# Kernel optimization log

Measured on AMD Instinct MI355X. Metric: run time of the kernel, lower is better.

Reference implementation:

```python
import jax, jax.numpy as jnp
import numpy as np

KS = 3          # deformable kernel size
N = KS * KS     # sampling points per output location


def conv2d(x, w, stride, pad):
    return jax.lax.conv_general_dilated(
        x, w, (stride, stride), [(pad, pad), (pad, pad)],
        dimension_numbers=('NCHW', 'OIHW', 'NCHW'))


def bn_train(x, g, b, eps=1e-5):
    # training-mode BatchNorm2d: per-channel batch statistics (biased var)
    m = jnp.mean(x, axis=(0, 2, 3), keepdims=True)
    v = jnp.var(x, axis=(0, 2, 3), keepdims=True)
    return (x - m) * jax.lax.rsqrt(v + eps) * g.reshape(1, -1, 1, 1) + b.reshape(1, -1, 1, 1)


def gather_xq(xpad, qx, qy):
    # xpad: (b,c,Hp,Wp); qx,qy: (b,h,w,N) int32 -> (b,c,h,w,N)
    b, c, Hp, Wp = xpad.shape
    _, h, w, n = qx.shape
    idx = (qx * Wp + qy).reshape(b, 1, h * w * n)
    xf = xpad.reshape(b, c, Hp * Wp)
    out = jnp.take_along_axis(xf, jnp.broadcast_to(idx, (b, c, h * w * n)), axis=2)
    return out.reshape(b, c, h, w, n)


def deform_conv(x, Wp, bp, Wd):
    # self-contained DeformConv2D (deform-conv-v2 style, no modulation)
    b, c, h, w = x.shape
    offset = conv2d(x, Wp, 1, 1) + bp.reshape(1, -1, 1, 1)      # (b,2N,h,w)
    off = jnp.transpose(offset, (0, 2, 3, 1))                    # (b,h,w,2N)
    xpad = jnp.pad(x, ((0, 0), (0, 0), (1, 1), (1, 1)))          # zero_padding(1)
    Hpad, Wpad = h + 2, w + 2
    r = KS // 2
    pn_x = jnp.repeat(jnp.arange(-r, r + 1, dtype=x.dtype), KS)  # [-1,-1,-1,0,0,0,1,1,1]
    pn_y = jnp.tile(jnp.arange(-r, r + 1, dtype=x.dtype), KS)    # [-1,0,1,...]
    # sampling coords in padded image: p = p0 + pn + offset
    px = off[..., :N] + jnp.arange(1, h + 1, dtype=x.dtype)[None, :, None, None] + pn_x
    py = off[..., N:] + jnp.arange(1, w + 1, dtype=x.dtype)[None, None, :, None] + pn_y
    fx = jnp.floor(jax.lax.stop_gradient(px))
    fy = jnp.floor(jax.lax.stop_gradient(py))
    q_ltx = jnp.clip(fx, 0, Hpad - 1).astype(jnp.int32)
    q_lty = jnp.clip(fy, 0, Wpad - 1).astype(jnp.int32)
    q_rbx = jnp.clip(fx + 1, 0, Hpad - 1).astype(jnp.int32)
    q_rby = jnp.clip(fy + 1, 0, Wpad - 1).astype(jnp.int32)
    pxc = jnp.clip(px, 0, Hpad - 1)
    pyc = jnp.clip(py, 0, Wpad - 1)
    g_lt = (1 + (q_ltx - pxc)) * (1 + (q_lty - pyc))
    g_rb = (1 - (q_rbx - pxc)) * (1 - (q_rby - pyc))
    g_lb = (1 + (q_ltx - pxc)) * (1 - (q_rby - pyc))
    g_rt = (1 - (q_rbx - pxc)) * (1 + (q_lty - pyc))
    x_off = (g_lt[:, None] * gather_xq(xpad, q_ltx, q_lty)
           + g_rb[:, None] * gather_xq(xpad, q_rbx, q_rby)
           + g_lb[:, None] * gather_xq(xpad, q_ltx, q_rby)
           + g_rt[:, None] * gather_xq(xpad, q_rbx, q_lty))    # (b,c,h,w,N)
    # _reshape_x_offset: (b,c,h,w,kx,ky) -> (b,c,h*ks,w*ks)
    x_off = x_off.reshape(b, c, h, w, KS, KS).transpose(0, 1, 2, 4, 3, 5).reshape(b, c, h * KS, w * KS)
    return conv2d(x_off, Wd, KS, 0)                              # stride=ks conv


def setup_inputs() -> dict:
    key = jax.random.key(0)
    ks = jax.random.split(key, 8)
    def w(k, shape, fan):
        return jax.random.normal(k, shape, jnp.float32) * np.float32(1.0 / np.sqrt(fan))
    B = 2048
    return dict(
        x=jax.random.normal(ks[0], (B, 3, 4, 4), jnp.float32),
        W1=w(ks[1], (32, 3, 3, 3), 27),
        g1=jnp.ones(32, jnp.float32), b1=jnp.zeros(32, jnp.float32),
        W2=w(ks[2], (64, 32, 3, 3), 288),
        g2=jnp.ones(64, jnp.float32), b2=jnp.zeros(64, jnp.float32),
        W3=w(ks[3], (128, 64, 3, 3), 576),
        g3=jnp.ones(128, jnp.float32), b3=jnp.zeros(128, jnp.float32),
        Wp=w(ks[4], (18, 128, 3, 3), 1152) * np.float32(0.1),
        bp=jnp.zeros(18, jnp.float32),
        Wd=w(ks[5], (128, 128, 3, 3), 1152),
        g4=jnp.ones(128, jnp.float32), b4=jnp.zeros(128, jnp.float32),
        Wc=w(ks[6], (10, 128), 128),
        bc=jnp.zeros(10, jnp.float32),
    )


def reference(x, W1, g1, b1, W2, g2, b2, W3, g3, b3, Wp, bp, Wd, g4, b4, Wc, bc):
    x = bn_train(jax.nn.relu(conv2d(x, W1, 1, 1)), g1, b1)
    x = bn_train(jax.nn.relu(conv2d(x, W2, 1, 1)), g2, b2)
    x = bn_train(jax.nn.relu(conv2d(x, W3, 1, 1)), g3, b3)
    x = bn_train(jax.nn.relu(deform_conv(x, Wp, bp, Wd)), g4, b4)
    x = jnp.mean(x, axis=(2, 3))  # avg_pool2d(kernel=4) on 4x4 -> 1x1, then flatten
    return x @ Wc.T + bc
```

## Files before the change

### kernel.cpp

```cpp
#include <hip/hip_runtime.h>

#define NB 2048
#define CNT 32768.0f

#define OFF_Y1   0
#define OFF_Y2   524288
#define OFF_Y3   1572864
#define OFF_MEAN 3670016
#define OFF_ST   3932160
#define OFF_W2P  3933184
#define OFF_W3P  3942400
#define OFF_WPP  3979264
#define OFF_WDP  3997696

typedef __attribute__((ext_vector_type(8))) short bf16x8;
typedef __attribute__((ext_vector_type(4))) float f32x4;

__device__ __forceinline__ unsigned short f2bf(float f) {
  union { float f; unsigned int u; } v; v.f = f;
  unsigned int r = v.u + 0x7FFFu + ((v.u >> 16) & 1u);
  return (unsigned short)(r >> 16);
}
__device__ __forceinline__ float bf2f(unsigned short u) {
  union { unsigned int u; float f; } v; v.u = ((unsigned int)u) << 16;
  return v.f;
}

__device__ __forceinline__ void packw_one(const float* __restrict__ w, unsigned short* __restrict__ wpk,
                                          int CI, int CO, int NT, int i) {
  int KST = CI >> 5;
  int j = i & 7, l = (i >> 3) & 63, sn = i >> 9;
  int nt = sn % NT, step = sn / NT;
  int tap = step / KST, ks = step - tap * KST;
  int ci = ks * 32 + (l >> 4) * 8 + j, co = nt * 16 + (l & 15);
  wpk[i] = (co < CO) ? f2bf(w[(co * CI + ci) * 9 + tap]) : (unsigned short)0;
}

__device__ __forceinline__ void packwd_one(const float* __restrict__ Wd, unsigned short* __restrict__ wdp, int i) {
  int co = i / 1152, k = i % 1152;
  int tt = k >> 5, kk = k & 31, g = kk >> 3, j = kk & 7;
  int n = k >> 7, ci = k & 127;
  int nt = co >> 4, cc = co & 15, l = g * 16 + cc;
  wdp[((tt * 8 + nt) * 64 + l) * 8 + j] = f2bf(Wd[co * 1152 + ci * 9 + n]);
}

__global__ __launch_bounds__(256) void k_pre(const float* __restrict__ W2, const float* __restrict__ W3,
                                             const float* __restrict__ Wp, const float* __restrict__ Wd,
                                             unsigned short* __restrict__ w2p, unsigned short* __restrict__ w3p,
                                             unsigned short* __restrict__ wpp, unsigned short* __restrict__ wdp,
                                             const float* __restrict__ x, const float* __restrict__ W1,
                                             unsigned short* __restrict__ y1, float* __restrict__ st) {
  __shared__ float xs[384];
  __shared__ float w1s[864];
  __shared__ float sst[64];
  int t = threadIdx.x;
  if (blockIdx.x < 270) {
#pragma unroll
    for (int ii = 0; ii < 4; ++ii) {
      int i = blockIdx.x * 1024 + ii * 256 + t;
      if (i < 18432) packw_one(W2, w2p, 32, 64, 4, i);
      else if (i < 92160) packw_one(W3, w3p, 64, 128, 8, i - 18432);
      else if (i < 129024) packw_one(Wp, wpp, 128, 18, 2, i - 92160);
      else if (i < 276480) packwd_one(Wd, wdp, i - 129024);
    }
    return;
  }
  int b0 = (blockIdx.x - 270) * 8;
  if (t < 128) { xs[t] = x[b0 * 48 + t]; xs[256 + t] = x[b0 * 48 + 256 + t]; }
  else if (t < 256) xs[t] = x[b0 * 48 + t];
  for (int i = t; i < 864; i += 256) w1s[i] = W1[i];
  if (t < 64) sst[t] = 0.f;
  __syncthreads();
  for (int r = 0; r < 2; ++r) {
    int o = t + r * 256;
    int co = o >> 4, p = o & 15, h = p >> 2, w = p & 3;
    float s1 = 0.f, s2 = 0.f;
#pragma unroll
    for (int img = 0; img < 8; ++img) {
      float acc = 0.f;
      for (int ci = 0; ci < 3; ++ci) {
#pragma unroll
        for (int kx = 0; kx < 3; ++kx) {
          int ih = h + kx - 1;
          if (ih < 0 || ih > 3) continue;
#pragma unroll
          for (int ky = 0; ky < 3; ++ky) {
            int iw = w + ky - 1;
            if (iw < 0 || iw > 3) continue;
            acc += w1s[co * 27 + ci * 9 + kx * 3 + ky] * xs[img * 48 + ci * 16 + ih * 4 + iw];
          }
        }
      }
      acc = fmaxf(acc, 0.f);
      y1[(b0 + img) * 512 + o] = f2bf(acc);
      s1 += acc; s2 += acc * acc;
    }
    atomicAdd(&sst[co], s1);
    atomicAdd(&sst[32 + co], s2);
  }
  __syncthreads();
  if (t < 64) atomicAdd(&st[(t < 32) ? t : (96 + t)], sst[t]);
}

template <int CI, int CO>
__global__ __launch_bounds__(512, 4) void k_convm(const unsigned short* __restrict__ yin,
                                                  const unsigned short* __restrict__ wpk,
                                                  const float* __restrict__ stp,
                                                  const float* __restrict__ gp,
                                                  const float* __restrict__ bpar,
                                                  unsigned short* __restrict__ yout, float* __restrict__ stout) {
  constexpr int KST = CI / 32, NSTEP = 9 * KST, NT = CO / 16;
  constexpr int STR = (CI == 64) ? 72 : 40;
  constexpr int NCH = (NT == 8) ? 8 : 4;
  __shared__ __align__(16) unsigned short xnT[8][36 * STR];
  __shared__ float cst[4][CO * 16];
  __shared__ float scS[2 * CI];
  __shared__ float sst[2 * CO];
  int b0 = blockIdx.x * 8, t = threadIdx.x;
  uint4 z = {0u, 0u, 0u, 0u};
  for (int i = t; i < (8 * 36 * STR) / 8; i += 512) ((uint4*)xnT)[i] = z;
  if (t < CI) {
    float m = stp[t] / CNT;
    float v = stp[128 + t] / CNT - m * m;
    float s = gp[t] * rsqrtf(fmaxf(v, 0.f) + 1e-5f);
    scS[t] = s; scS[CI + t] = bpar[t] - m * s;
  }
  if (t < 2 * CO) sst[t] = 0.f;
  __syncthreads();
  for (int i = t; i < 8 * CI * 16; i += 512) {
    int img = i / (CI * 16), r = i - img * (CI * 16);
    int c = r >> 4, p = r & 15, h = p >> 2, w = p & 3;
    float v = bf2f(yin[(b0 + img) * CI * 16 + r]) * scS[c] + scS[CI + c];
    xnT[img][((h + 1) * 6 + (w + 1)) * STR + c] = f2bf(v);
  }
  __syncthreads();
  int wv = t >> 6, l = t & 63, px = l & 15, g = l >> 4, cc = l & 15;
  int h = px >> 2, w = px & 3;
  int wq = (NT == 8) ? wv : (wv & 3);
  int ib = (NT == 8) ? 0 : ((wv >> 2) * 4);
  f32x4 acc[NCH];
#pragma unroll
  for (int e = 0; e < NCH; ++e) acc[e] = f32x4{0.f, 0.f, 0.f, 0.f};
#pragma unroll
  for (int step = 0; step < NSTEP; ++step) {
    int tap = step / KST, ks = step - tap * KST;
    int kx = tap / 3, ky = tap % 3;
    bf16x8 bb = *(const bf16x8*)&wpk[((step * NT + wq) * 64 + l) * 8];
    int woff = ((h + kx) * 6 + (w + ky)) * STR + ks * 32 + g * 8;
#pragma unroll
    for (int e = 0; e < NCH; ++e) {
      bf16x8 a = *(const bf16x8*)&xnT[ib + e][woff];
      acc[e] = __builtin_amdgcn_mfma_f32_16x16x32_bf16(a, bb, acc[e], 0, 0, 0);
    }
  }
#pragma unroll
  for (int p = 0; p < 2; ++p) {
    if (NT == 8) {
#pragma unroll
      for (int e = 0; e < 4; ++e) {
        int co = wq * 16 + cc;
#pragma unroll
        for (int r = 0; r < 4; ++r) cst[e][co * 16 + (g * 4 + r)] = acc[4 * p + e][r];
      }
    } else {
      if ((wv >> 2) == p) {
#pragma unroll
        for (int e = 0; e < 4; ++e) {
          int co = wq * 16 + cc;
#pragma unroll
          for (int r = 0; r < 4; ++r) cst[e][co * 16 + (g * 4 + r)] = acc[e][r];
        }
      }
    }
    __syncthreads();
    if (NT == 8) {
      int ime = t >> 7, c = t & 127;
      float s1 = 0.f, s2 = 0.f;
      union { unsigned short u16[16]; uint4 u4[2]; } pk;
#pragma unroll
      for (int e = 0; e < 16; ++e) {
        float v = fmaxf(cst[ime][c * 16 + e], 0.f);
        pk.u16[e] = f2bf(v);
        s1 += v; s2 += v * v;
      }
      unsigned short* dst = &yout[(b0 + 4 * p + ime) * CO * 16 + c * 16];
      *(uint4*)dst = pk.u4[0];
      *(uint4*)(dst + 8) = pk.u4[1];
      atomicAdd(&sst[c], s1);
      atomicAdd(&sst[CO + c], s2);
    } else {
      int ime = t >> 7, tl = t & 127;
      int c = tl >> 1, e0 = (t & 1) * 8;
      float s1 = 0.f, s2 = 0.f;
      union { unsigned short u16[8]; uint4 u4; } pk;
#pragma unroll
      for (int e = 0; e < 8; ++e) {
        float v = fmaxf(cst[ime][c * 16 + e0 + e], 0.f);
        pk.u16[e] = f2bf(v);
        s1 += v; s2 += v * v;
      }
      *(uint4*)&yout[(b0 + 4 * p + ime) * CO * 16 + c * 16 + e0] = pk.u4;
      atomicAdd(&sst[c], s1);
      atomicAdd(&sst[CO + c], s2);
    }
    __syncthreads();
  }
  if (t < 2 * CO) atomicAdd(&stout[(t < CO) ? t : (128 - CO + t)], sst[t]);
}

__global__ __launch_bounds__(512, 4) void k_deform(const unsigned short* __restrict__ y3,
                                                   const unsigned short* __restrict__ wppk,
                                                   const float* __restrict__ bp,
                                                   const unsigned short* __restrict__ wdp,
                                                   const float* __restrict__ stp,
                                                   const float* __restrict__ gp,
                                                   const float* __restrict__ bpar,
                                                   float* __restrict__ meanw, float* __restrict__ stout) {
  __shared__ __align__(16) unsigned char smem[51712];
  unsigned short* xnb2 = (unsigned short*)smem;
  unsigned short* xnT  = (unsigned short*)(smem + 8192);
  unsigned short* sAT  = (unsigned short*)(smem + 8192);
  unsigned short* xoffA = (unsigned short*)(smem + 31232);
  float* cscr = (float*)(smem + 31232);
  float* scS  = (float*)(smem + 49664);
  float* sst  = (float*)(smem + 50688);
  int b0 = blockIdx.x * 2, t = threadIdx.x;
  uint4 z = {0u, 0u, 0u, 0u};
  for (int i = t; i < 1224; i += 512) ((uint4*)xnT)[i] = z;
  if (t < 128) {
    float m = stp[t] / CNT;
    float v = stp[128 + t] / CNT - m * m;
    float s = gp[t] * rsqrtf(fmaxf(v, 0.f) + 1e-5f);
    scS[t] = s; scS[128 + t] = bpar[t] - m * s;
  }
  if (t < 256) sst[t] = 0.f;
  __syncthreads();
  for (int i = t; i < 4096; i += 512) {
    int img = i >> 11, r = i & 2047;
    int c = r >> 4, p = r & 15, h = p >> 2, w = p & 3;
    float v = bf2f(y3[(b0 + img) * 2048 + r]) * scS[c] + scS[128 + c];
    unsigned short bv = f2bf(v);
    xnb2[img * 2048 + c * 16 + p] = bv;
    xnT[img * 4896 + ((h + 1) * 6 + (w + 1)) * 136 + c] = bv;
  }
  __syncthreads();
  int wv = t >> 6, l = t & 63, px = l & 15, g = l >> 4, cc = l & 15;
  int h = px >> 2, w = px & 3;
  {
    int imo = wv >> 2, half = (wv >> 1) & 1, nt = wv & 1;
    f32x4 oa = {0.f, 0.f, 0.f, 0.f};
#pragma unroll
    for (int si = 0; si < 18; ++si) {
      int s2 = half * 18 + si;
      int tap = s2 >> 2, ks = s2 & 3;
      int kx = tap / 3, ky = tap % 3;
      bf16x8 a = *(const bf16x8*)&xnT[imo * 4896 + ((h + kx) * 6 + (w + ky)) * 136 + ks * 32 + g * 8];
      bf16x8 bb = *(const bf16x8*)&wppk[((s2 * 2 + nt) * 64 + l) * 8];
      oa = __builtin_amdgcn_mfma_f32_16x16x32_bf16(a, bb, oa, 0, 0, 0);
    }
#pragma unroll
    for (int r = 0; r < 4; ++r) cscr[wv * 256 + (g * 4 + r) * 16 + px] = oa[r];
  }
  __syncthreads();
  if (t < 288) {
    int imo = t / 144, r = t - imo * 144;
    int p = r / 9, n = r % 9;
    int hh = p >> 2, ww = p & 3;
    int o1 = n, o2 = 9 + n;
    int nt1 = o1 >> 4, c1 = o1 & 15;
    int nt2 = o2 >> 4, c2 = o2 & 15;
    float off1 = bp[o1] + cscr[(imo * 4 + nt1) * 256 + p * 16 + c1]
               + cscr[(imo * 4 + 2 + nt1) * 256 + p * 16 + c1];
    float off2 = bp[o2] + cscr[(imo * 4 + nt2) * 256 + p * 16 + c2]
               + cscr[(imo * 4 + 2 + nt2) * 256 + p * 16 + c2];
    float sx = off1 + (float)(hh + 1) + (float)(n / 3 - 1);
    float sy = off2 + (float)(ww + 1) + (float)(n % 3 - 1);
    float fx = floorf(sx), fy = floorf(sy);
    float qlx = fminf(fmaxf(fx, 0.f), 5.f);
    float qly = fminf(fmaxf(fy, 0.f), 5.f);
    float qrx = fminf(fmaxf(fx + 1.f, 0.f), 5.f);
    float qry = fminf(fmaxf(fy + 1.f, 0.f), 5.f);
    float pxc = fminf(fmaxf(sx, 0.f), 5.f);
    float pyc = fminf(fmaxf(sy, 0.f), 5.f);
    float glt = (1.f + (qlx - pxc)) * (1.f + (qly - pyc));
    float grb = (1.f - (qrx - pxc)) * (1.f - (qry - pyc));
    float glb = (1.f + (qlx - pxc)) * (1.f - (qry - pyc));
    float grt = (1.f - (qrx - pxc)) * (1.f + (qly - pyc));
    int ilx = (int)qlx, ily = (int)qly, irx = (int)qrx, iry = (int)qry;
    int rowb = imo * 5760 + (n * 16 + p) * 40;
    uint4* rp = (uint4*)&sAT[rowb];
    rp[0] = z; rp[1] = z; rp[2] = z; rp[3] = z; rp[4] = z;
    auto PUT = [&](int qx, int qy, float gv) {
      if (qx >= 1 && qx <= 4 && qy >= 1 && qy <= 4)
        sAT[rowb + (qx - 1) * 4 + (qy - 1)] = f2bf(gv);
    };
    PUT(ilx, ily, glt);
    PUT(irx, iry, grb);
    PUT(ilx, iry, glb);
    PUT(irx, ily, grt);
  }
  __syncthreads();
  f32x4 acc0 = {0.f, 0.f, 0.f, 0.f};
  f32x4 acc1 = {0.f, 0.f, 0.f, 0.f};
  for (int ph = 0; ph < 4; ++ph) {
    for (int m = wv; m < 36; m += 8) {
      int imo = m / 18, mm = m - imo * 18;
      int ttl = mm >> 1;
      int tt = ph * 9 + ttl;
      int q = tt & 3, n = tt >> 2;
      int ct = 2 * q + (mm & 1);
      bf16x8 a = *(const bf16x8*)&xnb2[imo * 2048 + (ct * 16 + cc) * 16 + g * 8];
      bf16x8 bS = *(const bf16x8*)&sAT[imo * 5760 + (n * 16 + cc) * 40 + g * 8];
      f32x4 d = __builtin_amdgcn_mfma_f32_16x16x32_bf16(a, bS, f32x4{0.f, 0.f, 0.f, 0.f}, 0, 0, 0);
      int gp2 = (ct & 1) * 2 + (g >> 1);
      unsigned lo = (unsigned)f2bf(d[0]) | ((unsigned)f2bf(d[1]) << 16);
      unsigned hi = (unsigned)f2bf(d[2]) | ((unsigned)f2bf(d[3]) << 16);
      *(uint2*)&xoffA[imo * 4608 + (ttl * 64 + gp2 * 16 + cc) * 8 + (g & 1) * 4] = (uint2){lo, hi};
    }
    __syncthreads();
    __builtin_amdgcn_s_setprio(1);
#pragma unroll
    for (int ti = 0; ti < 9; ++ti) {
      bf16x8 bb = *(const bf16x8*)&wdp[(((ph * 9 + ti) * 8 + wv) * 64 + l) * 8];
      bf16x8 a0 = *(const bf16x8*)&xoffA[(ti * 64 + l) * 8];
      bf16x8 a1 = *(const bf16x8*)&xoffA[4608 + (ti * 64 + l) * 8];
      acc0 = __builtin_amdgcn_mfma_f32_16x16x32_bf16(a0, bb, acc0, 0, 0, 0);
      acc1 = __builtin_amdgcn_mfma_f32_16x16x32_bf16(a1, bb, acc1, 0, 0, 0);
    }
    __builtin_amdgcn_s_setprio(0);
    __syncthreads();
  }
  {
    float s1a = 0.f, s2a = 0.f, s1b = 0.f, s2b = 0.f;
#pragma unroll
    for (int r = 0; r < 4; ++r) {
      float v0 = fmaxf(acc0[r], 0.f);
      float v1 = fmaxf(acc1[r], 0.f);
      s1a += v0; s2a += v0 * v0;
      s1b += v1; s2b += v1 * v1;
    }
    s1a += __shfl_xor(s1a, 16); s1a += __shfl_xor(s1a, 32);
    s2a += __shfl_xor(s2a, 16); s2a += __shfl_xor(s2a, 32);
    s1b += __shfl_xor(s1b, 16); s1b += __shfl_xor(s1b, 32);
    s2b += __shfl_xor(s2b, 16); s2b += __shfl_xor(s2b, 32);
    if (g == 0) {
      int co = wv * 16 + cc;
      meanw[b0 * 128 + co] = s1a;
      meanw[(b0 + 1) * 128 + co] = s1b;
      atomicAdd(&sst[co], s1a + s1b);
      atomicAdd(&sst[128 + co], s2a + s2b);
    }
  }
  __syncthreads();
  if (t < 256) atomicAdd(&stout[t], sst[t]);
}

__global__ __launch_bounds__(256) void k_final(const float* __restrict__ mean,
                                               const float* __restrict__ stp,
                                               const float* __restrict__ gp,
                                               const float* __restrict__ bpar,
                                               const float* __restrict__ Wc, const float* __restrict__ bc,
                                               float* __restrict__ out) {
  __shared__ float wf[1280];
  __shared__ float scS[256];
  __shared__ float tb[10];
  int t = threadIdx.x;
  if (t < 128) {
    float m = stp[t] / CNT;
    float v = stp[128 + t] / CNT - m * m;
    float s = gp[t] * rsqrtf(fmaxf(v, 0.f) + 1e-5f);
    scS[t] = s; scS[128 + t] = bpar[t] - m * s;
  }
  __syncthreads();
  for (int i = t; i < 1280; i += 256) {
    int c = i & 127;
    wf[i] = Wc[i] * scS[c] * 0.0625f;
  }
  __syncthreads();
  if (t < 10) {
    float s = bc[t];
    for (int c = 0; c < 128; ++c) s += Wc[t * 128 + c] * scS[128 + c];
    tb[t] = s;
  }
  __syncthreads();
  int gidx = blockIdx.x * 256 + t;
  int img = gidx / 10, o = gidx - img * 10;
  const float* mr = mean + img * 128;
  const float* wr = wf + o * 128;
  float acc = tb[o];
#pragma unroll 8
  for (int c = 0; c < 128; ++c) acc += wr[c] * mr[c];
  out[gidx] = acc;
}

extern "C" void kernel_launch(void* const* d_in, const int* in_sizes, int n_in,
                              void* d_out, int out_size, void* d_ws, size_t ws_size,
                              hipStream_t stream) {
  const float* x  = (const float*)d_in[0];
  const float* W1 = (const float*)d_in[1];
  const float* g1 = (const float*)d_in[2];
  const float* b1 = (const float*)d_in[3];
  const float* W2 = (const float*)d_in[4];
  const float* g2 = (const float*)d_in[5];
  const float* b2 = (const float*)d_in[6];
  const float* W3 = (const float*)d_in[7];
  const float* g3 = (const float*)d_in[8];
  const float* b3 = (const float*)d_in[9];
  const float* Wp = (const float*)d_in[10];
  const float* bp = (const float*)d_in[11];
  const float* Wd = (const float*)d_in[12];
  const float* g4 = (const float*)d_in[13];
  const float* b4 = (const float*)d_in[14];
  const float* Wc = (const float*)d_in[15];
  const float* bc = (const float*)d_in[16];
  float* ws = (float*)d_ws;
  float* out = (float*)d_out;

  hipMemsetAsync(ws + OFF_ST, 0, 1024 * sizeof(float), stream);
  k_pre<<<526, 256, 0, stream>>>(W2, W3, Wp, Wd,
                                 (unsigned short*)(ws + OFF_W2P), (unsigned short*)(ws + OFF_W3P),
                                 (unsigned short*)(ws + OFF_WPP), (unsigned short*)(ws + OFF_WDP),
                                 x, W1, (unsigned short*)(ws + OFF_Y1), ws + OFF_ST);
  k_convm<32, 64><<<NB / 8, 512, 0, stream>>>((const unsigned short*)(ws + OFF_Y1),
                                              (const unsigned short*)(ws + OFF_W2P),
                                              ws + OFF_ST, g1, b1,
                                              (unsigned short*)(ws + OFF_Y2), ws + OFF_ST + 256);
  k_convm<64, 128><<<NB / 8, 512, 0, stream>>>((const unsigned short*)(ws + OFF_Y2),
                                               (const unsigned short*)(ws + OFF_W3P),
                                               ws + OFF_ST + 256, g2, b2,
                                               (unsigned short*)(ws + OFF_Y3), ws + OFF_ST + 512);
  k_deform<<<NB / 2, 512, 0, stream>>>((const unsigned short*)(ws + OFF_Y3),
                                       (const unsigned short*)(ws + OFF_WPP), bp,
                                       (const unsigned short*)(ws + OFF_WDP),
                                       ws + OFF_ST + 512, g3, b3, ws + OFF_MEAN, ws + OFF_ST + 768);
  k_final<<<80, 256, 0, stream>>>(ws + OFF_MEAN, ws + OFF_ST + 768, g4, b4, Wc, bc, out);
}
```

Measured before the change: 120.1 us.

## Split deform conv into offset kernel and GEMM kernel with 4 images per block

The fused deformable-conv kernel is split into two kernels. k_offs normalizes y3, computes offsets and bilinear sampling matrices for 4 images per block, and writes the normalized activations and sampling matrices to global workspace. k_dgemm reloads them and runs the deformable GEMM on 4 images per block, so each Wd weight fragment is reused across 4 accumulators instead of 2. The goal is to cut weight-load traffic per image and free LDS, at the cost of an extra global round trip for the intermediates and one more launch.

```diff
diff --git a/kernel.cpp b/kernel.cpp
--- a/kernel.cpp
+++ b/kernel.cpp
@@ -6,12 +6,14 @@
 #define OFF_Y1   0
 #define OFF_Y2   524288
 #define OFF_Y3   1572864
-#define OFF_MEAN 3670016
-#define OFF_ST   3932160
-#define OFF_W2P  3933184
-#define OFF_W3P  3942400
-#define OFF_WPP  3979264
-#define OFF_WDP  3997696
+#define OFF_XNB  3670016
+#define OFF_SAT  5767168
+#define OFF_MEAN 10485760
+#define OFF_ST   10747904
+#define OFF_W2P  10748928
+#define OFF_W3P  10758144
+#define OFF_WPP  10795008
+#define OFF_WDP  10813440
 
 typedef __attribute__((ext_vector_type(8))) short bf16x8;
 typedef __attribute__((ext_vector_type(4))) float f32x4;
@@ -208,73 +210,64 @@
   if (t < 2 * CO) atomicAdd(&stout[(t < CO) ? t : (128 - CO + t)], sst[t]);
 }
 
-__global__ __launch_bounds__(512, 4) void k_deform(const unsigned short* __restrict__ y3,
-                                                   const unsigned short* __restrict__ wppk,
-                                                   const float* __restrict__ bp,
-                                                   const unsigned short* __restrict__ wdp,
-                                                   const float* __restrict__ stp,
-                                                   const float* __restrict__ gp,
-                                                   const float* __restrict__ bpar,
-                                                   float* __restrict__ meanw, float* __restrict__ stout) {
-  __shared__ __align__(16) unsigned char smem[51712];
-  unsigned short* xnb2 = (unsigned short*)smem;
-  unsigned short* xnT  = (unsigned short*)(smem + 8192);
-  unsigned short* sAT  = (unsigned short*)(smem + 8192);
-  unsigned short* xoffA = (unsigned short*)(smem + 31232);
-  float* cscr = (float*)(smem + 31232);
-  float* scS  = (float*)(smem + 49664);
-  float* sst  = (float*)(smem + 50688);
-  int b0 = blockIdx.x * 2, t = threadIdx.x;
+__global__ __launch_bounds__(512, 4) void k_offs(const unsigned short* __restrict__ y3,
+                                                 const unsigned short* __restrict__ wppk,
+                                                 const float* __restrict__ bp,
+                                                 const float* __restrict__ stp,
+                                                 const float* __restrict__ gp,
+                                                 const float* __restrict__ bpar,
+                                                 unsigned short* __restrict__ xnbG,
+                                                 unsigned short* __restrict__ satG) {
+  __shared__ __align__(16) unsigned char smem[44800];
+  unsigned short* xnT = (unsigned short*)smem;
+  float* offs = (float*)(smem + 39168);
+  float* scS  = (float*)(smem + 43776);
+  int b0 = blockIdx.x * 4, t = threadIdx.x;
   uint4 z = {0u, 0u, 0u, 0u};
-  for (int i = t; i < 1224; i += 512) ((uint4*)xnT)[i] = z;
+  for (int i = t; i < 2448; i += 512) ((uint4*)xnT)[i] = z;
   if (t < 128) {
     float m = stp[t] / CNT;
     float v = stp[128 + t] / CNT - m * m;
     float s = gp[t] * rsqrtf(fmaxf(v, 0.f) + 1e-5f);
     scS[t] = s; scS[128 + t] = bpar[t] - m * s;
   }
-  if (t < 256) sst[t] = 0.f;
-  __syncthreads();
-  for (int i = t; i < 4096; i += 512) {
+  __syncthreads();
+  for (int i = t; i < 8192; i += 512) {
     int img = i >> 11, r = i & 2047;
     int c = r >> 4, p = r & 15, h = p >> 2, w = p & 3;
-    float v = bf2f(y3[(b0 + img) * 2048 + r]) * scS[c] + scS[128 + c];
+    float v = bf2f(y3[b0 * 2048 + i]) * scS[c] + scS[128 + c];
     unsigned short bv = f2bf(v);
-    xnb2[img * 2048 + c * 16 + p] = bv;
     xnT[img * 4896 + ((h + 1) * 6 + (w + 1)) * 136 + c] = bv;
+    xnbG[b0 * 2048 + i] = bv;
   }
   __syncthreads();
   int wv = t >> 6, l = t & 63, px = l & 15, g = l >> 4, cc = l & 15;
   int h = px >> 2, w = px & 3;
   {
-    int imo = wv >> 2, half = (wv >> 1) & 1, nt = wv & 1;
+    int img = wv >> 1, nt = wv & 1;
     f32x4 oa = {0.f, 0.f, 0.f, 0.f};
 #pragma unroll
-    for (int si = 0; si < 18; ++si) {
-      int s2 = half * 18 + si;
+    for (int s2 = 0; s2 < 36; ++s2) {
       int tap = s2 >> 2, ks = s2 & 3;
       int kx = tap / 3, ky = tap % 3;
-      bf16x8 a = *(const bf16x8*)&xnT[imo * 4896 + ((h + kx) * 6 + (w + ky)) * 136 + ks * 32 + g * 8];
+      bf16x8 a = *(const bf16x8*)&xnT[img * 4896 + ((h + kx) * 6 + (w + ky)) * 136 + ks * 32 + g * 8];
       bf16x8 bb = *(const bf16x8*)&wppk[((s2 * 2 + nt) * 64 + l) * 8];
       oa = __builtin_amdgcn_mfma_f32_16x16x32_bf16(a, bb, oa, 0, 0, 0);
     }
-#pragma unroll
-    for (int r = 0; r < 4; ++r) cscr[wv * 256 + (g * 4 + r) * 16 + px] = oa[r];
-  }
-  __syncthreads();
-  if (t < 288) {
-    int imo = t / 144, r = t - imo * 144;
+    int o = nt * 16 + cc;
+    if (o < 18) {
+      float bo = bp[o];
+#pragma unroll
+      for (int r = 0; r < 4; ++r) offs[img * 288 + o * 16 + (g * 4 + r)] = oa[r] + bo;
+    }
+  }
+  __syncthreads();
+  for (int s = t; s < 576; s += 512) {
+    int imo = s / 144, r = s - imo * 144;
     int p = r / 9, n = r % 9;
     int hh = p >> 2, ww = p & 3;
-    int o1 = n, o2 = 9 + n;
-    int nt1 = o1 >> 4, c1 = o1 & 15;
-    int nt2 = o2 >> 4, c2 = o2 & 15;
-    float off1 = bp[o1] + cscr[(imo * 4 + nt1) * 256 + p * 16 + c1]
-               + cscr[(imo * 4 + 2 + nt1) * 256 + p * 16 + c1];
-    float off2 = bp[o2] + cscr[(imo * 4 + nt2) * 256 + p * 16 + c2]
-               + cscr[(imo * 4 + 2 + nt2) * 256 + p * 16 + c2];
-    float sx = off1 + (float)(hh + 1) + (float)(n / 3 - 1);
-    float sy = off2 + (float)(ww + 1) + (float)(n % 3 - 1);
+    float sx = offs[imo * 288 + n * 16 + p] + (float)(hh + 1) + (float)(n / 3 - 1);
+    float sy = offs[imo * 288 + (9 + n) * 16 + p] + (float)(ww + 1) + (float)(n % 3 - 1);
     float fx = floorf(sx), fy = floorf(sy);
     float qlx = fminf(fmaxf(fx, 0.f), 5.f);
     float qly = fminf(fmaxf(fy, 0.f), 5.f);
@@ -287,30 +280,48 @@
     float glb = (1.f + (qlx - pxc)) * (1.f - (qry - pyc));
     float grt = (1.f - (qrx - pxc)) * (1.f + (qly - pyc));
     int ilx = (int)qlx, ily = (int)qly, irx = (int)qrx, iry = (int)qry;
-    int rowb = imo * 5760 + (n * 16 + p) * 40;
-    uint4* rp = (uint4*)&sAT[rowb];
-    rp[0] = z; rp[1] = z; rp[2] = z; rp[3] = z; rp[4] = z;
+    unsigned short* row = &satG[((b0 + imo) * 144 + (n * 16 + p)) * 32];
+    uint4* rp = (uint4*)row;
+    rp[0] = z; rp[1] = z; rp[2] = z; rp[3] = z;
     auto PUT = [&](int qx, int qy, float gv) {
       if (qx >= 1 && qx <= 4 && qy >= 1 && qy <= 4)
-        sAT[rowb + (qx - 1) * 4 + (qy - 1)] = f2bf(gv);
+        row[(qx - 1) * 4 + (qy - 1)] = f2bf(gv);
     };
     PUT(ilx, ily, glt);
     PUT(irx, iry, grb);
     PUT(ilx, iry, glb);
     PUT(irx, ily, grt);
   }
-  __syncthreads();
-  f32x4 acc0 = {0.f, 0.f, 0.f, 0.f};
-  f32x4 acc1 = {0.f, 0.f, 0.f, 0.f};
+}
+
+__global__ __launch_bounds__(512, 4) void k_dgemm(const unsigned short* __restrict__ xnbG,
+                                                  const unsigned short* __restrict__ satG,
+                                                  const unsigned short* __restrict__ wdp,
+                                                  float* __restrict__ meanw, float* __restrict__ stout) {
+  __shared__ __align__(16) unsigned char smem[54336];
+  unsigned short* xnb2 = (unsigned short*)smem;
+  unsigned short* xoffA = (unsigned short*)(smem + 16416);
+  float* sst = (float*)(smem + 53312);
+  int b0 = blockIdx.x * 4, t = threadIdx.x;
+  uint4 z = {0u, 0u, 0u, 0u};
+  if (t < 256) sst[t] = 0.f;
+  if (t < 2) ((uint4*)(smem + 16384))[t] = z;
+  for (int i = t; i < 1024; i += 512)
+    ((uint4*)xnb2)[i] = ((const uint4*)&xnbG[b0 * 2048])[i];
+  __syncthreads();
+  int wv = t >> 6, l = t & 63, g = l >> 4, cc = l & 15;
+  f32x4 acc[4];
+#pragma unroll
+  for (int e = 0; e < 4; ++e) acc[e] = f32x4{0.f, 0.f, 0.f, 0.f};
   for (int ph = 0; ph < 4; ++ph) {
-    for (int m = wv; m < 36; m += 8) {
+    for (int m = wv; m < 72; m += 8) {
       int imo = m / 18, mm = m - imo * 18;
       int ttl = mm >> 1;
       int tt = ph * 9 + ttl;
       int q = tt & 3, n = tt >> 2;
       int ct = 2 * q + (mm & 1);
       bf16x8 a = *(const bf16x8*)&xnb2[imo * 2048 + (ct * 16 + cc) * 16 + g * 8];
-      bf16x8 bS = *(const bf16x8*)&sAT[imo * 5760 + (n * 16 + cc) * 40 + g * 8];
+      bf16x8 bS = *(const bf16x8*)&satG[((b0 + imo) * 144 + (n * 16 + cc)) * 32 + g * 8];
       f32x4 d = __builtin_amdgcn_mfma_f32_16x16x32_bf16(a, bS, f32x4{0.f, 0.f, 0.f, 0.f}, 0, 0, 0);
       int gp2 = (ct & 1) * 2 + (g >> 1);
       unsigned lo = (unsigned)f2bf(d[0]) | ((unsigned)f2bf(d[1]) << 16);
@@ -322,33 +333,38 @@
 #pragma unroll
     for (int ti = 0; ti < 9; ++ti) {
       bf16x8 bb = *(const bf16x8*)&wdp[(((ph * 9 + ti) * 8 + wv) * 64 + l) * 8];
-      bf16x8 a0 = *(const bf16x8*)&xoffA[(ti * 64 + l) * 8];
-      bf16x8 a1 = *(const bf16x8*)&xoffA[4608 + (ti * 64 + l) * 8];
-      acc0 = __builtin_amdgcn_mfma_f32_16x16x32_bf16(a0, bb, acc0, 0, 0, 0);
-      acc1 = __builtin_amdgcn_mfma_f32_16x16x32_bf16(a1, bb, acc1, 0, 0, 0);
+#pragma unroll
+      for (int e = 0; e < 4; ++e) {
+        bf16x8 a = *(const bf16x8*)&xoffA[e * 4608 + (ti * 64 + l) * 8];
+        acc[e] = __builtin_amdgcn_mfma_f32_16x16x32_bf16(a, bb, acc[e], 0, 0, 0);
+      }
     }
     __builtin_amdgcn_s_setprio(0);
     __syncthreads();
   }
   {
-    float s1a = 0.f, s2a = 0.f, s1b = 0.f, s2b = 0.f;
-#pragma unroll
-    for (int r = 0; r < 4; ++r) {
-      float v0 = fmaxf(acc0[r], 0.f);
-      float v1 = fmaxf(acc1[r], 0.f);
-      s1a += v0; s2a += v0 * v0;
-      s1b += v1; s2b += v1 * v1;
-    }
-    s1a += __shfl_xor(s1a, 16); s1a += __shfl_xor(s1a, 32);
-    s2a += __shfl_xor(s2a, 16); s2a += __shfl_xor(s2a, 32);
-    s1b += __shfl_xor(s1b, 16); s1b += __shfl_xor(s1b, 32);
-    s2b += __shfl_xor(s2b, 16); s2b += __shfl_xor(s2b, 32);
+    float s1[4], s2[4];
+#pragma unroll
+    for (int e = 0; e < 4; ++e) {
+      s1[e] = 0.f; s2[e] = 0.f;
+#pragma unroll
+      for (int r = 0; r < 4; ++r) {
+        float v = fmaxf(acc[e][r], 0.f);
+        s1[e] += v; s2[e] += v * v;
+      }
+      s1[e] += __shfl_xor(s1[e], 16); s1[e] += __shfl_xor(s1[e], 32);
+      s2[e] += __shfl_xor(s2[e], 16); s2[e] += __shfl_xor(s2[e], 32);
+    }
     if (g == 0) {
       int co = wv * 16 + cc;
-      meanw[b0 * 128 + co] = s1a;
-      meanw[(b0 + 1) * 128 + co] = s1b;
-      atomicAdd(&sst[co], s1a + s1b);
-      atomicAdd(&sst[128 + co], s2a + s2b);
+      float ts1 = 0.f, ts2 = 0.f;
+#pragma unroll
+      for (int e = 0; e < 4; ++e) {
+        meanw[(b0 + e) * 128 + co] = s1[e];
+        ts1 += s1[e]; ts2 += s2[e];
+      }
+      atomicAdd(&sst[co], ts1);
+      atomicAdd(&sst[128 + co], ts2);
     }
   }
   __syncthreads();
@@ -429,9 +445,13 @@
                                                (const unsigned short*)(ws + OFF_W3P),
                                                ws + OFF_ST + 256, g2, b2,
                                                (unsigned short*)(ws + OFF_Y3), ws + OFF_ST + 512);
-  k_deform<<<NB / 2, 512, 0, stream>>>((const unsigned short*)(ws + OFF_Y3),
-                                       (const unsigned short*)(ws + OFF_WPP), bp,
-                                       (const unsigned short*)(ws + OFF_WDP),
-                                       ws + OFF_ST + 512, g3, b3, ws + OFF_MEAN, ws + OFF_ST + 768);
+  k_offs<<<NB / 4, 512, 0, stream>>>((const unsigned short*)(ws + OFF_Y3),
+                                     (const unsigned short*)(ws + OFF_WPP), bp,
+                                     ws + OFF_ST + 512, g3, b3,
+                                     (unsigned short*)(ws + OFF_XNB), (unsigned short*)(ws + OFF_SAT));
+  k_dgemm<<<NB / 4, 512, 0, stream>>>((const unsigned short*)(ws + OFF_XNB),
+                                      (const unsigned short*)(ws + OFF_SAT),
+                                      (const unsigned short*)(ws + OFF_WDP),
+                                      ws + OFF_MEAN, ws + OFF_ST + 768);
   k_final<<<80, 256, 0, stream>>>(ws + OFF_MEAN, ws + OFF_ST + 768, g4, b4, Wc, bc, out);
 }
```

Measured after the change: 130.3 us. 8.5% more time.
